# Optimization experiments

Measured on AMD Instinct MI355X. Metric: run time of the kernel, lower is better.

Reference implementation:

```python
import jax, jax.numpy as jnp
import numpy as np

D = 1024
B = 16384

def setup_inputs() -> dict:
    key = jax.random.key(0)
    ks = jax.random.split(key, 8)
    s = 1.0 / np.sqrt(D)  # torch Linear default init scale (uniform), use scaled normal
    return {
        "f1": jax.random.normal(ks[0], (B, D), jnp.float32),
        "f2": jax.random.normal(ks[1], (B, D), jnp.float32),
        "Wq": jax.random.normal(ks[2], (D, D), jnp.float32) * s,
        "bq": jax.random.normal(ks[3], (D,), jnp.float32) * s,
        "Wk": jax.random.normal(ks[4], (D, D), jnp.float32) * s,
        "bk": jax.random.normal(ks[5], (D,), jnp.float32) * s,
        "Wv": jax.random.normal(ks[6], (D, D), jnp.float32) * s,
        "bv": jax.random.normal(ks[7], (D,), jnp.float32) * s,
    }

def reference(f1, f2, Wq, bq, Wk, bk, Wv, bv):
    d = f1.shape[-1]
    feats = jnp.stack([f1, f2], axis=1)          # [B, 2, D]
    # nn.Linear: y = x @ W.T + b
    Q = jnp.einsum("bsd,ed->bse", feats, Wq) + bq  # [B, 2, D]
    K = jnp.einsum("bsd,ed->bse", feats, Wk) + bk
    V = jnp.einsum("bsd,ed->bse", feats, Wv) + bv
    scores = jnp.einsum("bse,bte->bst", Q, K) / jnp.sqrt(jnp.asarray(d, feats.dtype))  # [B, 2, 2]
    attn = jax.nn.softmax(scores, axis=-1)
    attended = jnp.einsum("bst,btd->bsd", attn, V)  # [B, 2, D]
    return attended.sum(axis=1)                     # [B, D]
```

## Files before the change

kernel.cpp:

```cpp
#include <hip/hip_runtime.h>
#include <hip/hip_bf16.h>
#include <stdint.h>

typedef unsigned short u16;
typedef __bf16 bf16x8 __attribute__((ext_vector_type(8)));
typedef float f32x4 __attribute__((ext_vector_type(4)));

#define D_DIM 1024
#define B_ROWS 16384
#define M_ROWS 32768
#define BM 128
#define BN 128
#define BK 64

__device__ __forceinline__ u16 f2bs(float f) {
    union { float f; unsigned u; } v; v.f = f;
    unsigned r = v.u + 0x7FFFu + ((v.u >> 16) & 1u);
    return (u16)(r >> 16);
}
__device__ __forceinline__ float bs2f(unsigned bits16) {
    union { unsigned u; float f; } v; v.u = bits16 << 16;
    return v.f;
}
__device__ __forceinline__ float b8x(uint4 q, int e) {
    unsigned w[4] = {q.x, q.y, q.z, q.w};
    return bs2f((w[e >> 1] >> ((unsigned)(e & 1) * 16u)) & 0xFFFFu);
}
__device__ __forceinline__ uint2 pack4(float4 f) {
    uint2 r;
    r.x = (unsigned)f2bs(f.x) | ((unsigned)f2bs(f.y) << 16);
    r.y = (unsigned)f2bs(f.z) | ((unsigned)f2bs(f.w) << 16);
    return r;
}

#define GLD16(gsrc, ldst)                                                      \
    __builtin_amdgcn_global_load_lds(                                          \
        (const __attribute__((address_space(1))) void*)(gsrc),                 \
        (__attribute__((address_space(3))) void*)(ldst), 16, 0, 0)

#define MFMA16(a, b, c) __builtin_amdgcn_mfma_f32_16x16x32_bf16((a), (b), (c), 0, 0, 0)

__global__ __launch_bounds__(256) void prep_all(const float* __restrict__ f1,
                                                const float* __restrict__ f2,
                                                const float* __restrict__ Wq,
                                                const float* __restrict__ Wk,
                                                const float* __restrict__ Wv,
                                                const float* __restrict__ bq,
                                                const float* __restrict__ bk,
                                                u16* __restrict__ X,
                                                u16* __restrict__ WqT,
                                                u16* __restrict__ WkT,
                                                u16* __restrict__ Wvb,
                                                float* __restrict__ u,
                                                float* __restrict__ v,
                                                float* __restrict__ cbuf) {
    const int bid = blockIdx.x;
    if (bid < 2048) {
        const float* in = (bid < 1024) ? Wq : Wk;
        u16* out = (bid < 1024) ? WqT : WkT;
        const int b = bid & 1023;
        __shared__ float lds[32][33];
        const int tx = threadIdx.x & 31;
        const int ty = threadIdx.x >> 5;
        const int r0 = (b >> 5) * 32;
        const int c0 = (b & 31) * 32;
#pragma unroll
        for (int i = 0; i < 4; ++i) {
            int r = ty + i * 8;
            lds[r][tx] = in[(size_t)(r0 + r) * D_DIM + c0 + tx];
        }
        __syncthreads();
#pragma unroll
        for (int i = 0; i < 4; ++i) {
            int r = ty + i * 8;
            out[(size_t)(c0 + r) * D_DIM + r0 + tx] = f2bs(lds[tx][r]);
        }
    } else if (bid < 3072) {
        size_t base = ((size_t)(bid - 2048) * 256 + threadIdx.x) * 4;
        *(uint2*)(Wvb + base) = pack4(*(const float4*)(Wv + base));
    } else if (bid < 3104) {
        const int b = bid - 3072;
        const int dl = threadIdx.x & 31;
        const int fg = threadIdx.x >> 5;
        const int d  = b * 32 + dl;
        float au = 0.f, av = 0.f;
        const int f0 = fg * 128;
        for (int f = f0; f < f0 + 128; ++f) {
            au = fmaf(Wq[(size_t)f * D_DIM + d], bk[f], au);
            av = fmaf(Wk[(size_t)f * D_DIM + d], bq[f], av);
        }
        __shared__ float su[8][32], sv[8][32];
        su[fg][dl] = au; sv[fg][dl] = av;
        __syncthreads();
        if (fg == 0) {
            float a = 0.f, b2 = 0.f;
#pragma unroll
            for (int g = 0; g < 8; ++g) { a += su[g][dl]; b2 += sv[g][dl]; }
            u[d] = a; v[d] = b2;
        }
        if (b == 0) {
            __shared__ float red[256];
            float p = 0.f;
            for (int f = threadIdx.x; f < D_DIM; f += 256) p = fmaf(bq[f], bk[f], p);
            red[threadIdx.x] = p;
            __syncthreads();
            for (int s = 128; s; s >>= 1) {
                if (threadIdx.x < s) red[threadIdx.x] += red[threadIdx.x + s];
                __syncthreads();
            }
            if (threadIdx.x == 0) cbuf[0] = red[0];
        }
    } else if (bid < 11296) {
        size_t idx  = (size_t)(bid - 3104) * 256 + threadIdx.x;
        size_t base = idx * 8;
        size_t brow = base >> 10;
        size_t col  = base & 1023;
        float4 a = *(const float4*)(f1 + base);
        float4 b = *(const float4*)(f1 + base + 4);
        uint2 p0 = pack4(a), p1 = pack4(b);
        uint4 o; o.x = p0.x; o.y = p0.y; o.z = p1.x; o.w = p1.y;
        *(uint4*)(X + (2 * brow) * D_DIM + col) = o;
    } else {
        size_t idx  = (size_t)(bid - 11296) * 256 + threadIdx.x;
        size_t base = idx * 8;
        size_t brow = base >> 10;
        size_t col  = base & 1023;
        float4 a = *(const float4*)(f2 + base);
        float4 b = *(const float4*)(f2 + base + 4);
        uint2 p0 = pack4(a), p1 = pack4(b);
        uint4 o; o.x = p0.x; o.y = p0.y; o.z = p1.x; o.w = p1.y;
        *(uint4*)(X + (2 * brow + 1) * D_DIM + col) = o;
    }
}

__global__ __launch_bounds__(256, 3) void gemm_small(const u16* __restrict__ A,
                                                     const u16* __restrict__ W,
                                                     u16* __restrict__ C, int ncols) {
    constexpr int K = D_DIM;
    __shared__ u16 As[BM * BK];
    __shared__ u16 Bs[BN * BK];

    const int cpx  = gridDim.x >> 3;
    const int orig = (blockIdx.x & 7) * cpx + (blockIdx.x >> 3);
    const int nTn = ncols / BN;
    const int m0 = (orig / nTn) * BM, n0 = (orig % nTn) * BN;

    const int tid  = threadIdx.x;
    const int lane = tid & 63;
    const int wave = tid >> 6;
    const int wr = wave >> 1, wc = wave & 1;
    const int lr = lane & 15;
    const int kg = lane >> 4;

    f32x4 acc[4][4] = {};

    const int sr  = tid >> 3;
    const int scs = ((tid & 7) ^ ((tid >> 3) & 7)) * 8;
    const u16* aRow = A + (size_t)(m0 + sr) * K + scs;
    const u16* bRow = W + (size_t)(n0 + sr) * K + scs;
    u16* aDst = As + tid * 8;
    u16* bDst = Bs + tid * 8;

    for (int kt = 0; kt < K; kt += BK) {
#pragma unroll
        for (int i = 0; i < 4; ++i) {
            GLD16(aRow + (size_t)i * 32 * K + kt, aDst + i * 2048);
            GLD16(bRow + (size_t)i * 32 * K + kt, bDst + i * 2048);
        }
        __syncthreads();
#pragma unroll
        for (int kk = 0; kk < 2; ++kk) {
            bf16x8 af[4], bfr[4];
            const int kx = kk * 4 + kg;
#pragma unroll
            for (int mf = 0; mf < 4; ++mf) {
                const int R = wr * 64 + mf * 16 + lr;
                af[mf] = *(const bf16x8*)(As + R * 64 + ((kx ^ (R & 7)) * 8));
            }
#pragma unroll
            for (int nf = 0; nf < 4; ++nf) {
                const int S = wc * 64 + nf * 16 + lr;
                bfr[nf] = *(const bf16x8*)(Bs + S * 64 + ((kx ^ (S & 7)) * 8));
            }
#pragma unroll
            for (int mf = 0; mf < 4; ++mf)
#pragma unroll
                for (int nf = 0; nf < 4; ++nf)
                    acc[mf][nf] = MFMA16(af[mf], bfr[nf], acc[mf][nf]);
        }
        __syncthreads();
    }

    const int cr = (lane >> 4) * 4;
    const int cc = lane & 15;
#pragma unroll
    for (int mf = 0; mf < 4; ++mf)
#pragma unroll
        for (int nf = 0; nf < 4; ++nf) {
            int col = n0 + wc * 64 + nf * 16 + cc;
#pragma unroll
            for (int j = 0; j < 4; ++j) {
                int row = m0 + wr * 64 + mf * 16 + cr + j;
                C[(size_t)row * ncols + col] = f2bs(acc[mf][nf][j]);
            }
        }
}

template<int MODE>
__global__ __launch_bounds__(512, 2) void gemm8p(const u16* __restrict__ A,
                                                 const u16* __restrict__ W,
                                                 const float* __restrict__ bias,
                                                 u16* __restrict__ C,
                                                 float* __restrict__ out,
                                                 int ncols) {
    constexpr int K  = D_DIM;
    constexpr int NT = K / 64;
    __shared__ u16 L[65536];

    const int cpx  = gridDim.x >> 3;
    const int orig = (blockIdx.x & 7) * cpx + (blockIdx.x >> 3);
    const int nTn  = ncols >> 8;
    const int m0 = (orig / nTn) << 8, n0 = (orig % nTn) << 8;

    const int tid  = threadIdx.x;
    const int lane = tid & 63;
    const int wid  = tid >> 6;
    const int wm = wid >> 2, wn = wid & 3;
    const int lr = lane & 15;
    const int kg = lane >> 4;
    const int r7 = lr & 7;
    const int cx0 = ((0 + kg) ^ r7) * 8;
    const int cx1 = ((4 + kg) ^ r7) * 8;
    const int sS  = (wn & 1) * 64;

    const int rb  = tid >> 3;
    const int scs = ((tid & 7) ^ (rb & 7)) * 8;
    const u16* aB = A + (size_t)(m0 + rb) * K + scs;
    const u16* bB = W + (size_t)(n0 + rb) * K + scs;
    u16* aD = L + tid * 8;
    u16* bD = L + 32768 + tid * 8;

#define ST_HALF(tile, h)                                                       \
    {                                                                          \
        const int d_ = (tile) & 1;                                             \
        const size_t ko_ = (size_t)(tile) * 64;                                \
        if ((h) < 2) {                                                         \
            const u16* s_ = aB + (size_t)(h) * 128 * K + ko_;                  \
            u16* t_ = aD + (d_ * 2 + (h)) * 8192;                              \
            GLD16(s_, t_);                                                     \
            GLD16(s_ + (size_t)64 * K, t_ + 4096);                            \
        } else {                                                               \
            const u16* s_ = bB + (size_t)((h) - 2) * 128 * K + ko_;            \
            u16* t_ = bD + (d_ * 2 + ((h) - 2)) * 8192;                        \
            GLD16(s_, t_);                                                     \
            GLD16(s_ + (size_t)64 * K, t_ + 4096);                            \
        }                                                                      \
    }

    f32x4 acc[8][4] = {};
    bf16x8 af[8][2], bf[4][2];

#pragma unroll
    for (int h = 0; h < 4; ++h) ST_HALF(0, h);
#pragma unroll
    for (int h = 0; h < 4; ++h) ST_HALF(1, h);
    asm volatile("s_waitcnt vmcnt(8)" ::: "memory");
    __builtin_amdgcn_s_barrier();

#pragma unroll 2
    for (int t = 0; t < NT; ++t) {
        const int d = t & 1;
        const u16* Ab = L + (d * 2 + wm) * 8192;
        const u16* Bb = L + 32768 + (d * 2 + (wn >> 1)) * 8192;
        const bool more = (t + 2 < NT);

#pragma unroll
        for (int m = 0; m < 4; ++m) {
            const int R = m * 16 + lr;
            af[m][0] = *(const bf16x8*)(Ab + R * 64 + cx0);
            af[m][1] = *(const bf16x8*)(Ab + R * 64 + cx1);
        }
#pragma unroll
        for (int n = 0; n < 2; ++n) {
            const int S = sS + n * 16 + lr;
            bf[n][0] = *(const bf16x8*)(Bb + S * 64 + cx0);
            bf[n][1] = *(const bf16x8*)(Bb + S * 64 + cx1);
        }
        __builtin_amdgcn_s_barrier();
        __builtin_amdgcn_s_setprio(1);
#pragma unroll
        for (int m = 0; m < 4; ++m)
#pragma unroll
            for (int n = 0; n < 2; ++n) {
                acc[m][n] = MFMA16(af[m][0], bf[n][0], acc[m][n]);
                acc[m][n] = MFMA16(af[m][1], bf[n][1], acc[m][n]);
            }
        __builtin_amdgcn_s_setprio(0);
        __builtin_amdgcn_s_barrier();

#pragma unroll
        for (int n = 2; n < 4; ++n) {
            const int S = sS + n * 16 + lr;
            bf[n][0] = *(const bf16x8*)(Bb + S * 64 + cx0);
            bf[n][1] = *(const bf16x8*)(Bb + S * 64 + cx1);
        }
        __builtin_amdgcn_s_barrier();
        __builtin_amdgcn_s_setprio(1);
#pragma unroll
        for (int m = 0; m < 4; ++m)
#pragma unroll
            for (int n = 2; n < 4; ++n) {
                acc[m][n] = MFMA16(af[m][0], bf[n][0], acc[m][n]);
                acc[m][n] = MFMA16(af[m][1], bf[n][1], acc[m][n]);
            }
        __builtin_amdgcn_s_setprio(0);
        __builtin_amdgcn_s_barrier();

#pragma unroll
        for (int m = 4; m < 8; ++m) {
            const int R = m * 16 + lr;
            af[m][0] = *(const bf16x8*)(Ab + R * 64 + cx0);
            af[m][1] = *(const bf16x8*)(Ab + R * 64 + cx1);
        }
        if (more) { ST_HALF(t + 2, 2); ST_HALF(t + 2, 3); }
        __builtin_amdgcn_s_barrier();
        __builtin_amdgcn_s_setprio(1);
#pragma unroll
        for (int m = 4; m < 8; ++m)
#pragma unroll
            for (int n = 0; n < 2; ++n) {
                acc[m][n] = MFMA16(af[m][0], bf[n][0], acc[m][n]);
                acc[m][n] = MFMA16(af[m][1], bf[n][1], acc[m][n]);
            }
        __builtin_amdgcn_s_setprio(0);
        __builtin_amdgcn_s_barrier();

        if (more) { ST_HALF(t + 2, 0); ST_HALF(t + 2, 1); }
        __builtin_amdgcn_s_barrier();
        __builtin_amdgcn_s_setprio(1);
#pragma unroll
        for (int m = 4; m < 8; ++m)
#pragma unroll
            for (int n = 2; n < 4; ++n) {
                acc[m][n] = MFMA16(af[m][0], bf[n][0], acc[m][n]);
                acc[m][n] = MFMA16(af[m][1], bf[n][1], acc[m][n]);
            }
        __builtin_amdgcn_s_setprio(0);
        if (more) asm volatile("s_waitcnt vmcnt(8)" ::: "memory");
        else      asm volatile("s_waitcnt vmcnt(0)" ::: "memory");
        __builtin_amdgcn_s_barrier();
    }
#undef ST_HALF

    const int cr = (lane >> 4) * 4;
    const int cc = lane & 15;
    if constexpr (MODE == 0) {
#pragma unroll
        for (int mf = 0; mf < 8; ++mf)
#pragma unroll
            for (int nf = 0; nf < 4; ++nf) {
                int col = n0 + wn * 64 + nf * 16 + cc;
#pragma unroll
                for (int j = 0; j < 4; ++j) {
                    int row = m0 + wm * 128 + mf * 16 + cr + j;
                    C[(size_t)row * ncols + col] = f2bs(acc[mf][nf][j]);
                }
            }
    } else {
#pragma unroll
        for (int mf = 0; mf < 8; ++mf)
#pragma unroll
            for (int nf = 0; nf < 4; ++nf) {
                int col = n0 + wn * 64 + nf * 16 + cc;
                float bsv = 2.0f * bias[col];
#pragma unroll
                for (int j = 0; j < 4; ++j) {
                    int row = m0 + wm * 128 + mf * 16 + cr + j;
                    out[(size_t)row * ncols + col] = acc[mf][nf][j] + bsv;
                }
            }
    }
}

__global__ __launch_bounds__(256) void scores_z(const u16* __restrict__ X,
                                                const u16* __restrict__ G,
                                                const float* __restrict__ u,
                                                const float* __restrict__ v,
                                                const float* __restrict__ cbuf,
                                                u16* __restrict__ Z) {
    const int wave = threadIdx.x >> 6;
    const int lane = threadIdx.x & 63;
    const size_t b = (size_t)blockIdx.x * 4 + wave;
    const u16* x0p = X + (2 * b) * D_DIM;
    const u16* x1p = x0p + D_DIM;
    const u16* g0p = G + (2 * b) * D_DIM;
    const u16* g1p = g0p + D_DIM;

    float d00 = 0.f, d01 = 0.f, d10 = 0.f, d11 = 0.f;
    float au0 = 0.f, au1 = 0.f, bv0 = 0.f, bv1 = 0.f;
    uint4 x0c[2], x1c[2];
#pragma unroll
    for (int s = 0; s < 2; ++s) {
        const int c = s * 512 + lane * 8;
        x0c[s] = *(const uint4*)(x0p + c);
        x1c[s] = *(const uint4*)(x1p + c);
        uint4 g0 = *(const uint4*)(g0p + c);
        uint4 g1 = *(const uint4*)(g1p + c);
        float4 uuA = *(const float4*)(u + c);
        float4 uuB = *(const float4*)(u + c + 4);
        float4 vvA = *(const float4*)(v + c);
        float4 vvB = *(const float4*)(v + c + 4);
        float uA[8] = {uuA.x, uuA.y, uuA.z, uuA.w, uuB.x, uuB.y, uuB.z, uuB.w};
        float vA[8] = {vvA.x, vvA.y, vvA.z, vvA.w, vvB.x, vvB.y, vvB.z, vvB.w};
#pragma unroll
        for (int e = 0; e < 8; ++e) {
            float a0 = b8x(x0c[s], e), a1 = b8x(x1c[s], e);
            float c0 = b8x(g0, e),     c1 = b8x(g1, e);
            d00 = fmaf(a0, c0, d00); d01 = fmaf(a0, c1, d01);
            d10 = fmaf(a1, c0, d10); d11 = fmaf(a1, c1, d11);
            au0 = fmaf(uA[e], a0, au0); au1 = fmaf(uA[e], a1, au1);
            bv0 = fmaf(vA[e], a0, bv0); bv1 = fmaf(vA[e], a1, bv1);
        }
    }
#pragma unroll
    for (int off = 32; off; off >>= 1) {
        d00 += __shfl_xor(d00, off); d01 += __shfl_xor(d01, off);
        d10 += __shfl_xor(d10, off); d11 += __shfl_xor(d11, off);
        au0 += __shfl_xor(au0, off); au1 += __shfl_xor(au1, off);
        bv0 += __shfl_xor(bv0, off); bv1 += __shfl_xor(bv1, off);
    }
    const float cc0 = cbuf[0];
    const float sc = 1.0f / 32.0f;
    float s00 = (d00 + au0 + bv0 + cc0) * sc;
    float s01 = (d01 + au0 + bv1 + cc0) * sc;
    float s10 = (d10 + au1 + bv0 + cc0) * sc;
    float s11 = (d11 + au1 + bv1 + cc0) * sc;
    float mA = fmaxf(s00, s01);
    float e00 = expf(s00 - mA), e01 = expf(s01 - mA);
    float rA = 1.0f / (e00 + e01);
    float mB = fmaxf(s10, s11);
    float e10 = expf(s10 - mB), e11 = expf(s11 - mB);
    float rB = 1.0f / (e10 + e11);
    const float w0 = e00 * rA + e10 * rB;
    const float w1 = e01 * rA + e11 * rB;

#pragma unroll
    for (int s = 0; s < 2; ++s) {
        const int c = s * 512 + lane * 8;
        float4 lo, hi;
        lo.x = w0 * b8x(x0c[s], 0) + w1 * b8x(x1c[s], 0);
        lo.y = w0 * b8x(x0c[s], 1) + w1 * b8x(x1c[s], 1);
        lo.z = w0 * b8x(x0c[s], 2) + w1 * b8x(x1c[s], 2);
        lo.w = w0 * b8x(x0c[s], 3) + w1 * b8x(x1c[s], 3);
        hi.x = w0 * b8x(x0c[s], 4) + w1 * b8x(x1c[s], 4);
        hi.y = w0 * b8x(x0c[s], 5) + w1 * b8x(x1c[s], 5);
        hi.z = w0 * b8x(x0c[s], 6) + w1 * b8x(x1c[s], 6);
        hi.w = w0 * b8x(x0c[s], 7) + w1 * b8x(x1c[s], 7);
        uint2 pl = pack4(lo), ph = pack4(hi);
        uint4 o; o.x = pl.x; o.y = pl.y; o.z = ph.x; o.w = ph.y;
        *(uint4*)(Z + b * D_DIM + c) = o;
    }
}

extern "C" void kernel_launch(void* const* d_in, const int* in_sizes, int n_in,
                              void* d_out, int out_size, void* d_ws, size_t ws_size,
                              hipStream_t stream) {
    const float* f1 = (const float*)d_in[0];
    const float* f2 = (const float*)d_in[1];
    const float* Wq = (const float*)d_in[2];
    const float* bq = (const float*)d_in[3];
    const float* Wk = (const float*)d_in[4];
    const float* bk = (const float*)d_in[5];
    const float* Wv = (const float*)d_in[6];
    const float* bv = (const float*)d_in[7];
    float* out = (float*)d_out;

    char*   w    = (char*)d_ws;
    u16*    X    = (u16*)w;
    u16*    G    = X + (size_t)M_ROWS * D_DIM;
    u16*    Z    = G + (size_t)M_ROWS * D_DIM;
    u16*    Wvb  = Z + (size_t)B_ROWS * D_DIM;
    u16*    WqT  = Wvb + (size_t)D_DIM * D_DIM;
    u16*    WkT  = WqT + (size_t)D_DIM * D_DIM;
    u16*    Mb   = WkT + (size_t)D_DIM * D_DIM;
    float*  u    = (float*)(Mb + (size_t)D_DIM * D_DIM);
    float*  v    = u + D_DIM;
    float*  cbuf = v + D_DIM;

    prep_all<<<3104 + 2 * ((B_ROWS * D_DIM / 8) / 256), 256, 0, stream>>>(
        f1, f2, Wq, Wk, Wv, bq, bk, X, WqT, WkT, Wvb, u, v, cbuf);

    gemm_small<<<(D_DIM / BM) * (D_DIM / BN), 256, 0, stream>>>(WqT, WkT, Mb, D_DIM);
    gemm8p<0><<<(M_ROWS / 256) * (D_DIM / 256), 512, 0, stream>>>(
        X, Mb, nullptr, G, nullptr, D_DIM);
    scores_z<<<B_ROWS / 4, 256, 0, stream>>>(X, G, u, v, cbuf, Z);
    gemm8p<1><<<(B_ROWS / 256) * (D_DIM / 256), 512, 0, stream>>>(
        Z, Wvb, bv, nullptr, out, D_DIM);
}
```

Measured before the change: 197.5 us.

## Use narrower 256x128 tile GEMM kernel for final V projection

Replaces the templated 256x256-tile GEMM used for the final Z·Wv projection with a dedicated kernel using 256x128 tiles and a matching double-buffered LDS pipeline with 48K shared memory. This doubles the block count for the 16384-row GEMM (512 vs 256 blocks) to better fill the GPU's compute units and reduces LDS footprint. In exchange, it lowers per-block B-tile reuse and has more loads per MFMA.

```diff
diff --git a/kernel.cpp b/kernel.cpp
--- a/kernel.cpp
+++ b/kernel.cpp
@@ -206,12 +206,9 @@
         }
 }
 
-template<int MODE>
 __global__ __launch_bounds__(512, 2) void gemm8p(const u16* __restrict__ A,
                                                  const u16* __restrict__ W,
-                                                 const float* __restrict__ bias,
                                                  u16* __restrict__ C,
-                                                 float* __restrict__ out,
                                                  int ncols) {
     constexpr int K  = D_DIM;
     constexpr int NT = K / 64;
@@ -354,32 +351,165 @@
 
     const int cr = (lane >> 4) * 4;
     const int cc = lane & 15;
-    if constexpr (MODE == 0) {
-#pragma unroll
-        for (int mf = 0; mf < 8; ++mf)
-#pragma unroll
-            for (int nf = 0; nf < 4; ++nf) {
-                int col = n0 + wn * 64 + nf * 16 + cc;
-#pragma unroll
-                for (int j = 0; j < 4; ++j) {
-                    int row = m0 + wm * 128 + mf * 16 + cr + j;
-                    C[(size_t)row * ncols + col] = f2bs(acc[mf][nf][j]);
-                }
-            }
-    } else {
-#pragma unroll
-        for (int mf = 0; mf < 8; ++mf)
-#pragma unroll
-            for (int nf = 0; nf < 4; ++nf) {
-                int col = n0 + wn * 64 + nf * 16 + cc;
-                float bsv = 2.0f * bias[col];
-#pragma unroll
-                for (int j = 0; j < 4; ++j) {
-                    int row = m0 + wm * 128 + mf * 16 + cr + j;
-                    out[(size_t)row * ncols + col] = acc[mf][nf][j] + bsv;
-                }
-            }
-    }
+#pragma unroll
+    for (int mf = 0; mf < 8; ++mf)
+#pragma unroll
+        for (int nf = 0; nf < 4; ++nf) {
+            int col = n0 + wn * 64 + nf * 16 + cc;
+#pragma unroll
+            for (int j = 0; j < 4; ++j) {
+                int row = m0 + wm * 128 + mf * 16 + cr + j;
+                C[(size_t)row * ncols + col] = f2bs(acc[mf][nf][j]);
+            }
+        }
+}
+
+__global__ __launch_bounds__(512, 2) void gemm_v2(const u16* __restrict__ A,
+                                                  const u16* __restrict__ W,
+                                                  const float* __restrict__ bias,
+                                                  float* __restrict__ out) {
+    constexpr int K  = D_DIM;
+    constexpr int NT = K / 64;
+    __shared__ u16 L[49152];
+
+    const int cpx  = gridDim.x >> 3;
+    const int orig = (blockIdx.x & 7) * cpx + (blockIdx.x >> 3);
+    const int nTn  = 8;
+    const int m0 = (orig / nTn) * 256, n0 = (orig % nTn) * 128;
+
+    const int tid  = threadIdx.x;
+    const int lane = tid & 63;
+    const int wid  = tid >> 6;
+    const int wm = wid >> 2, wn = wid & 3;
+    const int lr = lane & 15;
+    const int kg = lane >> 4;
+    const int r7 = lr & 7;
+    const int cx0 = ((0 + kg) ^ r7) * 8;
+    const int cx1 = ((4 + kg) ^ r7) * 8;
+    const int sS  = wn * 32;
+
+    const int rb  = tid >> 3;
+    const int scs = ((tid & 7) ^ (rb & 7)) * 8;
+    const u16* aB = A + (size_t)(m0 + rb) * K + scs;
+    const u16* bB = W + (size_t)(n0 + rb) * K + scs;
+    u16* aD = L + tid * 8;
+    u16* bD = L + 32768 + tid * 8;
+
+#define ST_V(tile, h)                                                          \
+    {                                                                          \
+        const int d_ = (tile) & 1;                                             \
+        const size_t ko_ = (size_t)(tile) * 64;                                \
+        if ((h) < 2) {                                                         \
+            const u16* s_ = aB + (size_t)(h) * 128 * K + ko_;                  \
+            u16* t_ = aD + (d_ * 2 + (h)) * 8192;                              \
+            GLD16(s_, t_);                                                     \
+            GLD16(s_ + (size_t)64 * K, t_ + 4096);                            \
+        } else {                                                               \
+            u16* t_ = bD + d_ * 8192;                                          \
+            GLD16(bB + ko_, t_);                                               \
+            GLD16(bB + (size_t)64 * K + ko_, t_ + 4096);                      \
+        }                                                                      \
+    }
+
+    f32x4 acc[8][2] = {};
+    bf16x8 af[8][2], bf[2][2];
+
+#pragma unroll
+    for (int h = 0; h < 3; ++h) ST_V(0, h);
+#pragma unroll
+    for (int h = 0; h < 3; ++h) ST_V(1, h);
+    asm volatile("s_waitcnt vmcnt(6)" ::: "memory");
+    __builtin_amdgcn_s_barrier();
+
+#pragma unroll 2
+    for (int t = 0; t < NT; ++t) {
+        const int d = t & 1;
+        const u16* Ab = L + (d * 2 + wm) * 8192;
+        const u16* Bb = L + 32768 + d * 8192;
+        const bool more = (t + 2 < NT);
+
+#pragma unroll
+        for (int m = 0; m < 4; ++m) {
+            const int R = m * 16 + lr;
+            af[m][0] = *(const bf16x8*)(Ab + R * 64 + cx0);
+            af[m][1] = *(const bf16x8*)(Ab + R * 64 + cx1);
+        }
+        {
+            const int S = sS + lr;
+            bf[0][0] = *(const bf16x8*)(Bb + S * 64 + ((kg ^ (S & 7)) * 8));
+            bf[0][1] = *(const bf16x8*)(Bb + S * 64 + (((4 + kg) ^ (S & 7)) * 8));
+        }
+        __builtin_amdgcn_s_barrier();
+        __builtin_amdgcn_s_setprio(1);
+#pragma unroll
+        for (int m = 0; m < 4; ++m) {
+            acc[m][0] = MFMA16(af[m][0], bf[0][0], acc[m][0]);
+            acc[m][0] = MFMA16(af[m][1], bf[0][1], acc[m][0]);
+        }
+        __builtin_amdgcn_s_setprio(0);
+        __builtin_amdgcn_s_barrier();
+
+        {
+            const int S = sS + 16 + lr;
+            bf[1][0] = *(const bf16x8*)(Bb + S * 64 + ((kg ^ (S & 7)) * 8));
+            bf[1][1] = *(const bf16x8*)(Bb + S * 64 + (((4 + kg) ^ (S & 7)) * 8));
+        }
+        __builtin_amdgcn_s_barrier();
+        __builtin_amdgcn_s_setprio(1);
+#pragma unroll
+        for (int m = 0; m < 4; ++m) {
+            acc[m][1] = MFMA16(af[m][0], bf[1][0], acc[m][1]);
+            acc[m][1] = MFMA16(af[m][1], bf[1][1], acc[m][1]);
+        }
+        __builtin_amdgcn_s_setprio(0);
+        __builtin_amdgcn_s_barrier();
+
+#pragma unroll
+        for (int m = 4; m < 8; ++m) {
+            const int R = m * 16 + lr;
+            af[m][0] = *(const bf16x8*)(Ab + R * 64 + cx0);
+            af[m][1] = *(const bf16x8*)(Ab + R * 64 + cx1);
+        }
+        if (more) { ST_V(t + 2, 2); }
+        __builtin_amdgcn_s_barrier();
+        __builtin_amdgcn_s_setprio(1);
+#pragma unroll
+        for (int m = 4; m < 8; ++m) {
+            acc[m][0] = MFMA16(af[m][0], bf[0][0], acc[m][0]);
+            acc[m][0] = MFMA16(af[m][1], bf[0][1], acc[m][0]);
+        }
+        __builtin_amdgcn_s_setprio(0);
+        __builtin_amdgcn_s_barrier();
+
+        if (more) { ST_V(t + 2, 0); ST_V(t + 2, 1); }
+        __builtin_amdgcn_s_barrier();
+        __builtin_amdgcn_s_setprio(1);
+#pragma unroll
+        for (int m = 4; m < 8; ++m) {
+            acc[m][1] = MFMA16(af[m][0], bf[1][0], acc[m][1]);
+            acc[m][1] = MFMA16(af[m][1], bf[1][1], acc[m][1]);
+        }
+        __builtin_amdgcn_s_setprio(0);
+        if (more) asm volatile("s_waitcnt vmcnt(6)" ::: "memory");
+        else      asm volatile("s_waitcnt vmcnt(0)" ::: "memory");
+        __builtin_amdgcn_s_barrier();
+    }
+#undef ST_V
+
+    const int cr = (lane >> 4) * 4;
+    const int cc = lane & 15;
+#pragma unroll
+    for (int mf = 0; mf < 8; ++mf)
+#pragma unroll
+        for (int nf = 0; nf < 2; ++nf) {
+            int col = n0 + wn * 32 + nf * 16 + cc;
+            float bsv = 2.0f * bias[col];
+#pragma unroll
+            for (int j = 0; j < 4; ++j) {
+                int row = m0 + wm * 128 + mf * 16 + cr + j;
+                out[(size_t)row * D_DIM + col] = acc[mf][nf][j] + bsv;
+            }
+        }
 }
 
 __global__ __launch_bounds__(256) void scores_z(const u16* __restrict__ X,
@@ -491,9 +621,7 @@
         f1, f2, Wq, Wk, Wv, bq, bk, X, WqT, WkT, Wvb, u, v, cbuf);
 
     gemm_small<<<(D_DIM / BM) * (D_DIM / BN), 256, 0, stream>>>(WqT, WkT, Mb, D_DIM);
-    gemm8p<0><<<(M_ROWS / 256) * (D_DIM / 256), 512, 0, stream>>>(
-        X, Mb, nullptr, G, nullptr, D_DIM);
+    gemm8p<<<(M_ROWS / 256) * (D_DIM / 256), 512, 0, stream>>>(X, Mb, G, D_DIM);
     scores_z<<<B_ROWS / 4, 256, 0, stream>>>(X, G, u, v, cbuf, Z);
-    gemm8p<1><<<(B_ROWS / 256) * (D_DIM / 256), 512, 0, stream>>>(
-        Z, Wvb, bv, nullptr, out, D_DIM);
-}
+    gemm_v2<<<(B_ROWS / 256) * (D_DIM / 128), 512, 0, stream>>>(Z, Wvb, bv, out);
+}
```

Result: no change. 200.8 us (+1.7%).
